# Performance work log

Measured on AMD Instinct MI355X. Metric: run time of the kernel, lower is better.

Reference implementation:

```python
import jax, jax.numpy as jnp
import numpy as np

MIN_EXPERT_CAPACITY = 4
CAPACITY_FACTOR = 1.0


def setup_inputs() -> dict:
    key = jax.random.key(0)
    k0, k1, k2, k3 = jax.random.split(key, 4)
    B, S, D, E, F = 4, 2048, 1024, 8, 4096
    x = jax.random.normal(k0, (B, S, D), dtype=jnp.float32)
    router_w = jax.random.normal(k1, (D, E), dtype=jnp.float32) * (D ** -0.5)
    w1 = jax.random.normal(k2, (E, D, F), dtype=jnp.float32) * (D ** -0.5)
    b1 = jnp.zeros((E, F), dtype=jnp.float32)
    w2 = jax.random.normal(k3, (E, F, D), dtype=jnp.float32) * (F ** -0.5)
    b2 = jnp.zeros((E, D), dtype=jnp.float32)
    return {"x": x, "router_w": router_w, "w1": w1, "b1": b1, "w2": w2, "b2": b2}


def _moe_forward(x, router_w, w1, b1, w2, b2):
    B, S, D = x.shape
    E = router_w.shape[1]
    G = 1  # num_groups (single device -> all-to-all is identity)
    T = B * S  # tokens per group
    C = max(int(round(CAPACITY_FACTOR * T / E)), MIN_EXPERT_CAPACITY)

    xt = x.reshape(G, T, D)
    # ---- top-1 tokens-choose masked router ----
    logits = jnp.einsum('gtd,de->gte', xt, router_w)
    probs = jax.nn.softmax(logits, axis=-1)
    gate = jnp.max(probs, axis=-1)          # [g, t]
    idx = jnp.argmax(probs, axis=-1)        # [g, t]
    emask = jax.nn.one_hot(idx, E, dtype=x.dtype)  # [g, t, e]
    # position of each token within its chosen expert's buffer (0-based);
    # -1 for unselected slots -> one_hot gives zeros
    pos = jnp.cumsum(emask, axis=1) * emask - 1.0
    pos = pos.astype(jnp.int32)
    # drop tokens beyond capacity
    slot = jax.nn.one_hot(pos, C, dtype=x.dtype)   # [g, t, e, c]
    dispatch = emask[..., None] * slot             # [g, t, e, c] (0/1)
    combine = dispatch * gate[..., None, None]     # [g, t, e, c]

    # ---- dispatch / expert FFN / combine ----
    expert_inputs = jnp.einsum('gtd,gtec->gecd', xt, dispatch)        # [g, e, c, d]
    h = jax.nn.relu(jnp.einsum('gecd,edf->gecf', expert_inputs, w1) + b1[None, :, None, :])
    expert_outputs = jnp.einsum('gecf,efd->gecd', h, w2) + b2[None, :, None, :]
    out = jnp.einsum('gecd,gtec->gtd', expert_outputs, combine)       # [g, t, d]
    return out.reshape(B, S, D)


def reference(x, router_w, w1, b1, w2, b2):
    return _moe_forward(x, router_w, w1, b1, w2, b2)
```

## Files before the change

kernel.cpp:

```cpp
#include <hip/hip_runtime.h>
#include <hip/hip_fp16.h>

typedef unsigned short ushort_t;
typedef __attribute__((ext_vector_type(8))) _Float16 half8v;
typedef __attribute__((ext_vector_type(4))) float float4v;
typedef __attribute__((ext_vector_type(8))) unsigned short ushort8v;

#define DEV_INLINE __device__ __forceinline__

DEV_INLINE ushort_t f2h_bits(float f) {
  return __half_as_ushort(__float2half(f));
}

__global__ __launch_bounds__(256) void router_kernel(
    const float* __restrict__ x, const float* __restrict__ rw,
    int* __restrict__ idx, float* __restrict__ gate)
{
  constexpr int D = 1024, E = 8;
  int token = (int)((blockIdx.x * 256 + threadIdx.x) >> 6);
  int lane = threadIdx.x & 63;
  const float* xr = x + (size_t)token * D;
  float acc[E];
#pragma unroll
  for (int e = 0; e < E; ++e) acc[e] = 0.f;
  for (int d = lane; d < D; d += 64) {
    float xv = xr[d];
#pragma unroll
    for (int e = 0; e < E; ++e) acc[e] += xv * rw[d * E + e];
  }
#pragma unroll
  for (int off = 32; off >= 1; off >>= 1) {
#pragma unroll
    for (int e = 0; e < E; ++e) acc[e] += __shfl_xor(acc[e], off);
  }
  if (lane == 0) {
    float m = acc[0]; int am = 0;
#pragma unroll
    for (int e = 1; e < E; ++e) { if (acc[e] > m) { m = acc[e]; am = e; } }
    float s = 0.f;
#pragma unroll
    for (int e = 0; e < E; ++e) s += __expf(acc[e] - m);
    idx[token] = am;
    gate[token] = 1.0f / s;
  }
}

__global__ __launch_bounds__(1024) void scan_kernel(
    const int* __restrict__ idx,
    int* __restrict__ slotmap, int* __restrict__ tok2slot)
{
  constexpr int C = 1024, E = 8;
  __shared__ unsigned long long s0[1024];
  __shared__ unsigned long long s1[1024];
  int tid = threadIdx.x;
  int myidx[8];
  unsigned long long c0 = 0, c1 = 0;
#pragma unroll
  for (int j = 0; j < 8; ++j) {
    int e = idx[tid * 8 + j];
    myidx[j] = e;
    if (e < 4) c0 += 1ull << (16 * e);
    else       c1 += 1ull << (16 * (e - 4));
  }
  s0[tid] = c0; s1[tid] = c1;
  __syncthreads();
  for (int off = 1; off < 1024; off <<= 1) {
    unsigned long long b0 = 0, b1 = 0;
    if (tid >= off) { b0 = s0[tid - off]; b1 = s1[tid - off]; }
    __syncthreads();
    s0[tid] += b0; s1[tid] += b1;
    __syncthreads();
  }
  unsigned long long p0 = s0[tid] - c0, p1 = s1[tid] - c1;
  unsigned long long t0 = s0[1023], t1 = s1[1023];
  int cnt[E];
#pragma unroll
  for (int e = 0; e < 4; ++e) {
    cnt[e]     = (int)((p0 >> (16 * e)) & 0xFFFF);
    cnt[4 + e] = (int)((p1 >> (16 * e)) & 0xFFFF);
  }
#pragma unroll
  for (int j = 0; j < 8; ++j) {
    int t = tid * 8 + j;
    int e = myidx[j];
    int pos = cnt[e]++;
    if (pos < C) {
      slotmap[e * C + pos] = t;
      tok2slot[t] = e * C + pos;
    } else {
      tok2slot[t] = -1;
    }
  }
  int total[E];
#pragma unroll
  for (int e = 0; e < 4; ++e) {
    total[e]     = (int)((t0 >> (16 * e)) & 0xFFFF);
    total[4 + e] = (int)((t1 >> (16 * e)) & 0xFFFF);
  }
  for (int s = tid; s < E * C; s += 1024) {
    int e = s / C, c = s % C;
    if (c >= total[e]) slotmap[s] = -1;
  }
}

__global__ __launch_bounds__(256) void gather_kernel(
    const float* __restrict__ x, const int* __restrict__ slotmap,
    ushort_t* __restrict__ Xe)
{
  constexpr int D = 1024;
  int slot = blockIdx.x;
  int t = slotmap[slot];
  int tid = threadIdx.x;
  ushort4* dst = (ushort4*)(Xe + (size_t)slot * D);
  ushort4 o;
  if (t >= 0) {
    float4 v = ((const float4*)(x + (size_t)t * D))[tid];
    o.x = f2h_bits(v.x); o.y = f2h_bits(v.y); o.z = f2h_bits(v.z); o.w = f2h_bits(v.w);
  } else {
    o.x = 0; o.y = 0; o.z = 0; o.w = 0;
  }
  dst[tid] = o;
}

__global__ __launch_bounds__(256) void transpose_cvt(
    const float* __restrict__ in, ushort_t* __restrict__ out, int R, int Cc)
{
  __shared__ ushort_t tile[64][65];
  size_t base = (size_t)blockIdx.z * (size_t)R * (size_t)Cc;
  int c0 = blockIdx.x * 64, r0 = blockIdx.y * 64;
  int tx = threadIdx.x & 63, ty = threadIdx.x >> 6;
#pragma unroll
  for (int i = 0; i < 16; ++i) {
    int r = ty + 4 * i;
    tile[r][tx] = f2h_bits(in[base + (size_t)(r0 + r) * Cc + c0 + tx]);
  }
  __syncthreads();
#pragma unroll
  for (int i = 0; i < 2; ++i) {
    int chunk = (int)threadIdx.x + i * 256;
    int c = chunk >> 3, g = chunk & 7;
    ushort8v v;
#pragma unroll
    for (int j = 0; j < 8; ++j) v[j] = tile[8 * g + j][c];
    *(ushort8v*)(out + base + (size_t)(c0 + c) * R + r0 + 8 * g) = v;
  }
}

__global__ __launch_bounds__(256) void combine_kernel(
    const float* __restrict__ p, const float* __restrict__ b2,
    const int* __restrict__ tok2slot, const float* __restrict__ gate,
    float* __restrict__ out)
{
  constexpr int D = 1024;
  constexpr size_t ECD = (size_t)8 * 1024 * 1024;
  int t = blockIdx.x;
  int d4 = threadIdx.x;
  float4* o = (float4*)(out + (size_t)t * D);
  int slot = tok2slot[t];
  if (slot < 0) { o[d4] = make_float4(0.f, 0.f, 0.f, 0.f); return; }
  int e = slot >> 10;
  float g = gate[t];
  float4 a = ((const float4*)(p + (size_t)slot * D))[d4];
  float4 b = ((const float4*)(p + ECD + (size_t)slot * D))[d4];
  float4 bb = ((const float4*)(b2 + (size_t)e * D))[d4];
  o[d4] = make_float4((a.x + b.x + bb.x) * g, (a.y + b.y + bb.y) * g,
                      (a.z + b.z + bb.z) * g, (a.w + b.w + bb.w) * g);
}

#define BAR()  asm volatile("s_barrier" ::: "memory")
#define VM2()  asm volatile("s_waitcnt vmcnt(2)" ::: "memory")
#define VM4()  asm volatile("s_waitcnt vmcnt(4)" ::: "memory")
#define VM0()  asm volatile("s_waitcnt vmcnt(0)" ::: "memory")

#define RD_A0(buf) { _Pragma("unroll") for (int i_ = 0; i_ < 4; ++i_) { \
  _Pragma("unroll") for (int kh_ = 0; kh_ < 2; ++kh_) \
    aS0[i_][kh_] = *(const half8v*)&lds[buf][kh_*KH + (arow + i_*16)*32 + axor]; } }
#define RD_A1(buf) { _Pragma("unroll") for (int i_ = 0; i_ < 4; ++i_) { \
  _Pragma("unroll") for (int kh_ = 0; kh_ < 2; ++kh_) \
    aS1[i_][kh_] = *(const half8v*)&lds[buf][kh_*KH + (arow + (4+i_)*16)*32 + axor]; } }
#define RD_B0(buf) { _Pragma("unroll") for (int j_ = 0; j_ < 2; ++j_) { \
  _Pragma("unroll") for (int kh_ = 0; kh_ < 2; ++kh_) \
    bS0[j_][kh_] = *(const half8v*)&lds[buf][AELEM + kh_*KH + (brow + j_*16)*32 + axor]; } }
#define RD_B1(buf) { _Pragma("unroll") for (int j_ = 0; j_ < 2; ++j_) { \
  _Pragma("unroll") for (int kh_ = 0; kh_ < 2; ++kh_) \
    bS1[j_][kh_] = *(const half8v*)&lds[buf][AELEM + kh_*KH + (brow + (2+j_)*16)*32 + axor]; } }

#define MQ(AS, BS, MB, NB) { __builtin_amdgcn_s_setprio(1); \
  _Pragma("unroll") for (int i_ = 0; i_ < 4; ++i_) { \
  _Pragma("unroll") for (int j_ = 0; j_ < 2; ++j_) { \
    acc[(MB)+i_][(NB)+j_] = __builtin_amdgcn_mfma_f32_16x16x32_f16(AS[i_][0], BS[j_][0], acc[(MB)+i_][(NB)+j_], 0, 0, 0); \
    acc[(MB)+i_][(NB)+j_] = __builtin_amdgcn_mfma_f32_16x16x32_f16(AS[i_][1], BS[j_][1], acc[(MB)+i_][(NB)+j_], 0, 0, 0); } } \
  __builtin_amdgcn_s_setprio(0); }

template<int KFULL, int NTM, int NTN, int SK, int MODE>
__global__ __launch_bounds__(512, 2) void gemm8p(
    const ushort_t* __restrict__ A, const ushort_t* __restrict__ Bt,
    const float* __restrict__ bias,
    ushort_t* __restrict__ Hout, float* __restrict__ outp)
{
  constexpr int M_ = NTM * 256, N_ = NTN * 256;
  constexpr int KB = KFULL / SK;
  constexpr int NT = KB / 64;
  constexpr int NU = NT / 2;
  constexpr int KH = 256 * 32;
  constexpr int AELEM = 2 * KH;
  constexpr int WPB = NTM * NTN * SK;
  constexpr int NWG = 8 * WPB;
  constexpr int CPX = NWG / 8;

  __shared__ __attribute__((aligned(16))) ushort_t lds[2][2 * AELEM];

  const int bid = blockIdx.x;
  const int swz = (bid & 7) * CPX + (bid >> 3);
  const int e   = swz / WPB;
  int r = swz % WPB;
  const int sk  = r / (NTM * NTN);  r %= NTM * NTN;
  const int nt  = r / NTM;
  const int mt  = r % NTM;
  const int kb0 = sk * KB;

  const ushort_t* Ae = A  + (size_t)e * M_ * KFULL + (size_t)(mt * 256) * KFULL + kb0;
  const ushort_t* Be = Bt + (size_t)e * N_ * KFULL + (size_t)(nt * 256) * KFULL + kb0;

  const int tid  = threadIdx.x;
  const int lane = tid & 63;
  const int w    = tid >> 6;
  const int wr   = w >> 2;
  const int wc   = w & 3;
  const int l15  = lane & 15;
  const int axor = ((lane >> 4) ^ ((l15 >> 1) & 3)) << 3;
  const int arow = wr * 128 + l15;
  const int brow = wc * 64 + l15;

  const int srow = tid >> 2;
  const int su   = tid & 3;
  auto stage = [&](int buf, int isB, int h, int ktile) {
    const ushort_t* base = isB ? Be : Ae;
#pragma unroll
    for (int kh = 0; kh < 2; ++kh) {
      int row = h * 128 + srow;
      int ul  = su ^ ((row >> 1) & 3);
      const ushort_t* src = base + (size_t)row * KFULL + ktile * 64 + kh * 32 + ul * 8;
      __builtin_amdgcn_global_load_lds(
          (const __attribute__((address_space(1))) void*)src,
          (__attribute__((address_space(3))) void*)(&lds[buf][isB * AELEM + kh * KH + h * 4096 + tid * 8]),
          16, 0, 0);
    }
  };

  float4v acc[8][4] = {};
  half8v aS0[4][2], aS1[4][2], bS0[2][2], bS1[2][2];

  stage(0, 0, 0, 0); stage(0, 0, 1, 0); stage(0, 1, 0, 0); stage(0, 1, 1, 0);
  stage(1, 1, 0, 1); stage(1, 0, 0, 1);
  VM4(); BAR();
  RD_A0(0); RD_B0(0);

  for (int u = 0; u < NU - 1; ++u) {
    const int t1 = 2 * u + 1, t2 = 2 * u + 2, t3 = 2 * u + 3;
    RD_B1(0); stage(1, 0, 1, t1); BAR(); MQ(aS0, bS0, 0, 0); BAR();
    RD_A1(0); stage(1, 1, 1, t1); BAR(); MQ(aS0, bS1, 0, 2); VM2(); BAR();
    RD_A0(1); stage(0, 1, 0, t2); BAR(); MQ(aS1, bS0, 4, 0); VM2(); BAR();
    RD_B0(1); stage(0, 0, 0, t2); BAR(); MQ(aS1, bS1, 4, 2); BAR();
    RD_B1(1); stage(0, 0, 1, t2); BAR(); MQ(aS0, bS0, 0, 0); BAR();
    RD_A1(1); stage(0, 1, 1, t2); BAR(); MQ(aS0, bS1, 0, 2); VM2(); BAR();
    RD_A0(0); stage(1, 1, 0, t3); BAR(); MQ(aS1, bS0, 4, 0); VM2(); BAR();
    RD_B0(0); stage(1, 0, 0, t3); BAR(); MQ(aS1, bS1, 4, 2); BAR();
  }
  {
    const int t1 = NT - 1;
    RD_B1(0); stage(1, 0, 1, t1); BAR(); MQ(aS0, bS0, 0, 0); BAR();
    RD_A1(0); stage(1, 1, 1, t1); BAR(); MQ(aS0, bS1, 0, 2); VM2(); BAR();
    RD_A0(1);                     BAR(); MQ(aS1, bS0, 4, 0); VM0(); BAR();
    RD_B0(1);                     BAR(); MQ(aS1, bS1, 4, 2); BAR();
    RD_B1(1);                     BAR(); MQ(aS0, bS0, 0, 0); BAR();
    RD_A1(1);                     BAR(); MQ(aS0, bS1, 0, 2); BAR();
                                  BAR(); MQ(aS1, bS0, 4, 0); BAR();
                                         MQ(aS1, bS1, 4, 2);
  }

  const int lr4   = (lane >> 4) * 4;
  const int mbase = mt * 256 + wr * 128;
  const int nbase = nt * 256 + wc * 64;

  if (MODE == 0) {
    float bv[4];
#pragma unroll
    for (int j = 0; j < 4; ++j) bv[j] = bias[e * N_ + nbase + j * 16 + l15];
    ushort_t* He = Hout + (size_t)e * M_ * N_;
#pragma unroll
    for (int i = 0; i < 8; ++i) {
#pragma unroll
      for (int q = 0; q < 4; ++q) {
        int m = mbase + i * 16 + lr4 + q;
#pragma unroll
        for (int j = 0; j < 4; ++j) {
          float v = acc[i][j][q] + bv[j];
          v = v > 0.f ? v : 0.f;
          He[(size_t)m * N_ + nbase + j * 16 + l15] = f2h_bits(v);
        }
      }
    }
  } else {
    float* pe = outp + ((size_t)(sk * 8 + e)) * (size_t)M_ * N_;
#pragma unroll
    for (int i = 0; i < 8; ++i) {
#pragma unroll
      for (int q = 0; q < 4; ++q) {
        int m = mbase + i * 16 + lr4 + q;
#pragma unroll
        for (int j = 0; j < 4; ++j) {
          pe[(size_t)m * N_ + nbase + j * 16 + l15] = acc[i][j][q];
        }
      }
    }
  }
}

extern "C" void kernel_launch(void* const* d_in, const int* in_sizes, int n_in,
                              void* d_out, int out_size, void* d_ws, size_t ws_size,
                              hipStream_t stream)
{
  const float* x  = (const float*)d_in[0];
  const float* rw = (const float*)d_in[1];
  const float* w1 = (const float*)d_in[2];
  const float* b1 = (const float*)d_in[3];
  const float* w2 = (const float*)d_in[4];
  const float* b2 = (const float*)d_in[5];
  float* out = (float*)d_out;

  constexpr int D = 1024, E = 8, F = 4096, T = 8192, C = 1024;

  char* p = (char*)d_ws;
  auto take = [&](size_t bytes) { char* r = p; p += (bytes + 255) & ~(size_t)255; return r; };
  ushort_t* w1t = (ushort_t*)take((size_t)E * D * F * 2);
  ushort_t* w2t = (ushort_t*)take((size_t)E * F * D * 2);
  ushort_t* Xe  = (ushort_t*)take((size_t)E * C * D * 2);
  ushort_t* H   = (ushort_t*)take((size_t)E * C * F * 2);
  int*      idx = (int*)take((size_t)T * 4);
  float*   gate = (float*)take((size_t)T * 4);
  int*  slotmap = (int*)take((size_t)E * C * 4);
  int* tok2slot = (int*)take((size_t)T * 4);

  float* partials = (float*)w1t;

  router_kernel<<<T / 4, 256, 0, stream>>>(x, rw, idx, gate);
  scan_kernel<<<1, 1024, 0, stream>>>(idx, slotmap, tok2slot);
  gather_kernel<<<E * C, 256, 0, stream>>>(x, slotmap, Xe);
  transpose_cvt<<<dim3(F / 64, D / 64, E), 256, 0, stream>>>(w1, w1t, D, F);
  transpose_cvt<<<dim3(D / 64, F / 64, E), 256, 0, stream>>>(w2, w2t, F, D);
  gemm8p<1024, 4, 16, 1, 0><<<512, 512, 0, stream>>>(Xe, w1t, b1, H, nullptr);
  gemm8p<4096, 4, 4, 2, 1><<<256, 512, 0, stream>>>(H, w2t, nullptr, nullptr, partials);
  combine_kernel<<<T, 256, 0, stream>>>(partials, b2, tok2slot, gate, out);
}
```

Before: 284.1 us.

## Reschedule GEMM LDS prefetch pipeline and merge weight transpose launches

Reorders the GEMM main loop so each phase reads both the A and B fragments from LDS together, then spreads the global-to-LDS staging across the MFMA phases. The prologue now prefetches three stages, and the vmcnt waits are loosened to allow 4–6 loads in flight, with lgkmcnt waits added. The aim is to hide global load latency behind MFMA work and cut barrier stalls. The two weight transpose/convert launches are also merged into one kernel to save a launch and its tail, at the cost of more register pressure and a more fragile hand-tuned wait schedule.

```diff
diff --git a/kernel.cpp b/kernel.cpp
--- a/kernel.cpp
+++ b/kernel.cpp
@@ -122,12 +122,23 @@
   dst[tid] = o;
 }
 
-__global__ __launch_bounds__(256) void transpose_cvt(
-    const float* __restrict__ in, ushort_t* __restrict__ out, int R, int Cc)
+__global__ __launch_bounds__(256) void transpose_cvt2(
+    const float* __restrict__ w1, ushort_t* __restrict__ w1t,
+    const float* __restrict__ w2, ushort_t* __restrict__ w2t)
 {
   __shared__ ushort_t tile[64][65];
-  size_t base = (size_t)blockIdx.z * (size_t)R * (size_t)Cc;
-  int c0 = blockIdx.x * 64, r0 = blockIdx.y * 64;
+  int bb = blockIdx.x;
+  const float* in; ushort_t* out; int R, Cc, bx, by, bz;
+  if (bb < 8192) {
+    in = w1; out = w1t; R = 1024; Cc = 4096;
+    bz = bb >> 10; int rr = bb & 1023; bx = rr & 63; by = rr >> 6;
+  } else {
+    bb -= 8192;
+    in = w2; out = w2t; R = 4096; Cc = 1024;
+    bz = bb >> 10; int rr = bb & 1023; bx = rr & 15; by = rr >> 4;
+  }
+  size_t base = (size_t)bz * (size_t)R * (size_t)Cc;
+  int c0 = bx * 64, r0 = by * 64;
   int tx = threadIdx.x & 63, ty = threadIdx.x >> 6;
 #pragma unroll
   for (int i = 0; i < 16; ++i) {
@@ -167,10 +178,11 @@
                       (a.z + b.z + bb.z) * g, (a.w + b.w + bb.w) * g);
 }
 
-#define BAR()  asm volatile("s_barrier" ::: "memory")
-#define VM2()  asm volatile("s_waitcnt vmcnt(2)" ::: "memory")
-#define VM4()  asm volatile("s_waitcnt vmcnt(4)" ::: "memory")
-#define VM0()  asm volatile("s_waitcnt vmcnt(0)" ::: "memory")
+#define BAR()   asm volatile("s_barrier" ::: "memory")
+#define LGKM0() asm volatile("s_waitcnt lgkmcnt(0)" ::: "memory")
+#define VM4()   asm volatile("s_waitcnt vmcnt(4)" ::: "memory")
+#define VM6()   asm volatile("s_waitcnt vmcnt(6)" ::: "memory")
+#define VM0()   asm volatile("s_waitcnt vmcnt(0)" ::: "memory")
 
 #define RD_A0(buf) { _Pragma("unroll") for (int i_ = 0; i_ < 4; ++i_) { \
   _Pragma("unroll") for (int kh_ = 0; kh_ < 2; ++kh_) \
@@ -252,31 +264,41 @@
   half8v aS0[4][2], aS1[4][2], bS0[2][2], bS1[2][2];
 
   stage(0, 0, 0, 0); stage(0, 0, 1, 0); stage(0, 1, 0, 0); stage(0, 1, 1, 0);
-  stage(1, 1, 0, 1); stage(1, 0, 0, 1);
-  VM4(); BAR();
-  RD_A0(0); RD_B0(0);
+  stage(1, 0, 0, 1); stage(1, 0, 1, 1); stage(1, 1, 0, 1);
+  VM6(); BAR();
+  RD_B0(0); RD_A0(0);
 
   for (int u = 0; u < NU - 1; ++u) {
     const int t1 = 2 * u + 1, t2 = 2 * u + 2, t3 = 2 * u + 3;
-    RD_B1(0); stage(1, 0, 1, t1); BAR(); MQ(aS0, bS0, 0, 0); BAR();
-    RD_A1(0); stage(1, 1, 1, t1); BAR(); MQ(aS0, bS1, 0, 2); VM2(); BAR();
-    RD_A0(1); stage(0, 1, 0, t2); BAR(); MQ(aS1, bS0, 4, 0); VM2(); BAR();
-    RD_B0(1); stage(0, 0, 0, t2); BAR(); MQ(aS1, bS1, 4, 2); BAR();
-    RD_B1(1); stage(0, 0, 1, t2); BAR(); MQ(aS0, bS0, 0, 0); BAR();
-    RD_A1(1); stage(0, 1, 1, t2); BAR(); MQ(aS0, bS1, 0, 2); VM2(); BAR();
-    RD_A0(0); stage(1, 1, 0, t3); BAR(); MQ(aS1, bS0, 4, 0); VM2(); BAR();
-    RD_B0(0); stage(1, 0, 0, t3); BAR(); MQ(aS1, bS1, 4, 2); BAR();
+    RD_B1(0); RD_A1(0); stage(1, 1, 1, t1);
+    BAR(); MQ(aS0, bS0, 0, 0); LGKM0(); BAR();
+    stage(0, 0, 0, t2);
+    BAR(); MQ(aS0, bS1, 0, 2); BAR();
+    stage(0, 0, 1, t2);
+    BAR(); MQ(aS1, bS0, 4, 0); VM4(); BAR();
+    RD_B0(1); RD_A0(1); stage(0, 1, 0, t2);
+    BAR(); MQ(aS1, bS1, 4, 2); BAR();
+    RD_B1(1); RD_A1(1); stage(0, 1, 1, t2);
+    BAR(); MQ(aS0, bS0, 0, 0); LGKM0(); BAR();
+    stage(1, 0, 0, t3);
+    BAR(); MQ(aS0, bS1, 0, 2); BAR();
+    stage(1, 0, 1, t3);
+    BAR(); MQ(aS1, bS0, 4, 0); VM4(); BAR();
+    RD_B0(0); RD_A0(0); stage(1, 1, 0, t3);
+    BAR(); MQ(aS1, bS1, 4, 2); BAR();
   }
   {
-    const int t1 = NT - 1;
-    RD_B1(0); stage(1, 0, 1, t1); BAR(); MQ(aS0, bS0, 0, 0); BAR();
-    RD_A1(0); stage(1, 1, 1, t1); BAR(); MQ(aS0, bS1, 0, 2); VM2(); BAR();
-    RD_A0(1);                     BAR(); MQ(aS1, bS0, 4, 0); VM0(); BAR();
-    RD_B0(1);                     BAR(); MQ(aS1, bS1, 4, 2); BAR();
-    RD_B1(1);                     BAR(); MQ(aS0, bS0, 0, 0); BAR();
-    RD_A1(1);                     BAR(); MQ(aS0, bS1, 0, 2); BAR();
-                                  BAR(); MQ(aS1, bS0, 4, 0); BAR();
-                                         MQ(aS1, bS1, 4, 2);
+    RD_B1(0); RD_A1(0); stage(1, 1, 1, NT - 1);
+    BAR(); MQ(aS0, bS0, 0, 0); LGKM0(); BAR();
+    BAR(); MQ(aS0, bS1, 0, 2); BAR();
+    BAR(); MQ(aS1, bS0, 4, 0); VM0(); BAR();
+    RD_B0(1); RD_A0(1);
+    BAR(); MQ(aS1, bS1, 4, 2); BAR();
+    RD_B1(1); RD_A1(1);
+    BAR(); MQ(aS0, bS0, 0, 0); BAR();
+    BAR(); MQ(aS0, bS1, 0, 2); BAR();
+    BAR(); MQ(aS1, bS0, 4, 0); BAR();
+    MQ(aS1, bS1, 4, 2);
   }
 
   const int lr4   = (lane >> 4) * 4;
@@ -347,8 +369,7 @@
   router_kernel<<<T / 4, 256, 0, stream>>>(x, rw, idx, gate);
   scan_kernel<<<1, 1024, 0, stream>>>(idx, slotmap, tok2slot);
   gather_kernel<<<E * C, 256, 0, stream>>>(x, slotmap, Xe);
-  transpose_cvt<<<dim3(F / 64, D / 64, E), 256, 0, stream>>>(w1, w1t, D, F);
-  transpose_cvt<<<dim3(D / 64, F / 64, E), 256, 0, stream>>>(w2, w2t, F, D);
+  transpose_cvt2<<<16384, 256, 0, stream>>>(w1, w1t, w2, w2t);
   gemm8p<1024, 4, 16, 1, 0><<<512, 512, 0, stream>>>(Xe, w1t, b1, H, nullptr);
   gemm8p<4096, 4, 4, 2, 1><<<256, 512, 0, stream>>>(H, w2t, nullptr, nullptr, partials);
   combine_kernel<<<T, 256, 0, stream>>>(partials, b2, tok2slot, gate, out);
```

Result: faster. 277.6 us (-2.3%).

## Fuse weight fp32-to-fp16 transpose into GEMM B-tile loading

Applied to the files above, without the earlier changes.

Removes the two separate transpose_cvt kernels that converted and transposed w1 and w2 into fp16 workspace buffers. The GEMM now reads the fp32 weights directly through registers, converts them to fp16 and writes them transposed and swizzled into LDS, while A tiles still use direct global-to-LDS loads. The pipeline schedule is reworked around this register staging, with extra vmcnt(0) and lgkmcnt waits. This saves an extra full read and write pass over the weights, but the GEMM now reads twice as many bytes for B and adds VALU conversion and LDS-write work that may stall the MFMA pipeline.

```diff
diff --git a/kernel.cpp b/kernel.cpp
--- a/kernel.cpp
+++ b/kernel.cpp
@@ -10,6 +10,10 @@
 
 DEV_INLINE ushort_t f2h_bits(float f) {
   return __half_as_ushort(__float2half(f));
+}
+
+DEV_INLINE float comp4(const float4& q, int c) {
+  return c == 0 ? q.x : c == 1 ? q.y : c == 2 ? q.z : q.w;
 }
 
 __global__ __launch_bounds__(256) void router_kernel(
@@ -120,30 +124,6 @@
     o.x = 0; o.y = 0; o.z = 0; o.w = 0;
   }
   dst[tid] = o;
-}
-
-__global__ __launch_bounds__(256) void transpose_cvt(
-    const float* __restrict__ in, ushort_t* __restrict__ out, int R, int Cc)
-{
-  __shared__ ushort_t tile[64][65];
-  size_t base = (size_t)blockIdx.z * (size_t)R * (size_t)Cc;
-  int c0 = blockIdx.x * 64, r0 = blockIdx.y * 64;
-  int tx = threadIdx.x & 63, ty = threadIdx.x >> 6;
-#pragma unroll
-  for (int i = 0; i < 16; ++i) {
-    int r = ty + 4 * i;
-    tile[r][tx] = f2h_bits(in[base + (size_t)(r0 + r) * Cc + c0 + tx]);
-  }
-  __syncthreads();
-#pragma unroll
-  for (int i = 0; i < 2; ++i) {
-    int chunk = (int)threadIdx.x + i * 256;
-    int c = chunk >> 3, g = chunk & 7;
-    ushort8v v;
-#pragma unroll
-    for (int j = 0; j < 8; ++j) v[j] = tile[8 * g + j][c];
-    *(ushort8v*)(out + base + (size_t)(c0 + c) * R + r0 + 8 * g) = v;
-  }
 }
 
 __global__ __launch_bounds__(256) void combine_kernel(
@@ -167,10 +147,9 @@
                       (a.z + b.z + bb.z) * g, (a.w + b.w + bb.w) * g);
 }
 
-#define BAR()  asm volatile("s_barrier" ::: "memory")
-#define VM2()  asm volatile("s_waitcnt vmcnt(2)" ::: "memory")
-#define VM4()  asm volatile("s_waitcnt vmcnt(4)" ::: "memory")
-#define VM0()  asm volatile("s_waitcnt vmcnt(0)" ::: "memory")
+#define BAR()   asm volatile("s_barrier" ::: "memory")
+#define LGKM0() asm volatile("s_waitcnt lgkmcnt(0)" ::: "memory")
+#define VM0()   asm volatile("s_waitcnt vmcnt(0)" ::: "memory")
 
 #define RD_A0(buf) { _Pragma("unroll") for (int i_ = 0; i_ < 4; ++i_) { \
   _Pragma("unroll") for (int kh_ = 0; kh_ < 2; ++kh_) \
@@ -194,7 +173,7 @@
 
 template<int KFULL, int NTM, int NTN, int SK, int MODE>
 __global__ __launch_bounds__(512, 2) void gemm8p(
-    const ushort_t* __restrict__ A, const ushort_t* __restrict__ Bt,
+    const ushort_t* __restrict__ A, const float* __restrict__ Bf,
     const float* __restrict__ bias,
     ushort_t* __restrict__ Hout, float* __restrict__ outp)
 {
@@ -219,8 +198,8 @@
   const int mt  = r % NTM;
   const int kb0 = sk * KB;
 
-  const ushort_t* Ae = A  + (size_t)e * M_ * KFULL + (size_t)(mt * 256) * KFULL + kb0;
-  const ushort_t* Be = Bt + (size_t)e * N_ * KFULL + (size_t)(nt * 256) * KFULL + kb0;
+  const ushort_t* Ae = A + (size_t)e * M_ * KFULL + (size_t)(mt * 256) * KFULL + kb0;
+  const float*    Be = Bf + (size_t)e * KFULL * N_ + (size_t)kb0 * N_ + nt * 256;
 
   const int tid  = threadIdx.x;
   const int lane = tid & 63;
@@ -234,49 +213,90 @@
 
   const int srow = tid >> 2;
   const int su   = tid & 3;
-  auto stage = [&](int buf, int isB, int h, int ktile) {
-    const ushort_t* base = isB ? Be : Ae;
+  auto stageA = [&](int buf, int h, int ktile) {
 #pragma unroll
     for (int kh = 0; kh < 2; ++kh) {
       int row = h * 128 + srow;
       int ul  = su ^ ((row >> 1) & 3);
-      const ushort_t* src = base + (size_t)row * KFULL + ktile * 64 + kh * 32 + ul * 8;
+      const ushort_t* src = Ae + (size_t)row * KFULL + ktile * 64 + kh * 32 + ul * 8;
       __builtin_amdgcn_global_load_lds(
           (const __attribute__((address_space(1))) void*)src,
-          (__attribute__((address_space(3))) void*)(&lds[buf][isB * AELEM + kh * KH + h * 4096 + tid * 8]),
+          (__attribute__((address_space(3))) void*)(&lds[buf][kh * KH + h * 4096 + tid * 8]),
           16, 0, 0);
+    }
+  };
+
+  const int kqB   = tid & 15;
+  const int noctB = tid >> 4;
+  const int khB   = kqB >> 3;
+  const int guB   = (kqB >> 1) & 3;
+  const int hfB   = kqB & 1;
+  const int nb8   = noctB * 8;
+  float4 bf[8];
+  auto iB = [&](int ktile) {
+#pragma unroll
+    for (int kk = 0; kk < 4; ++kk)
+#pragma unroll
+      for (int nn = 0; nn < 2; ++nn)
+        bf[kk * 2 + nn] = *(const float4*)&Be[(size_t)(ktile * 64 + kqB * 4 + kk) * N_ + nb8 + nn * 4];
+  };
+  auto wB = [&](int buf) {
+#pragma unroll
+    for (int nn = 0; nn < 8; ++nn) {
+      const int n = nb8 + nn;
+      const int q = nn >> 2, c = nn & 3;
+      ushort4 wv;
+      wv.x = f2h_bits(comp4(bf[0 + q], c));
+      wv.y = f2h_bits(comp4(bf[2 + q], c));
+      wv.z = f2h_bits(comp4(bf[4 + q], c));
+      wv.w = f2h_bits(comp4(bf[6 + q], c));
+      *(ushort4*)&lds[buf][AELEM + khB * KH + n * 32 + ((guB ^ ((n >> 1) & 3)) << 3) + hfB * 4] = wv;
     }
   };
 
   float4v acc[8][4] = {};
   half8v aS0[4][2], aS1[4][2], bS0[2][2], bS1[2][2];
 
-  stage(0, 0, 0, 0); stage(0, 0, 1, 0); stage(0, 1, 0, 0); stage(0, 1, 1, 0);
-  stage(1, 1, 0, 1); stage(1, 0, 0, 1);
-  VM4(); BAR();
-  RD_A0(0); RD_B0(0);
-
-  for (int u = 0; u < NU - 1; ++u) {
-    const int t1 = 2 * u + 1, t2 = 2 * u + 2, t3 = 2 * u + 3;
-    RD_B1(0); stage(1, 0, 1, t1); BAR(); MQ(aS0, bS0, 0, 0); BAR();
-    RD_A1(0); stage(1, 1, 1, t1); BAR(); MQ(aS0, bS1, 0, 2); VM2(); BAR();
-    RD_A0(1); stage(0, 1, 0, t2); BAR(); MQ(aS1, bS0, 4, 0); VM2(); BAR();
-    RD_B0(1); stage(0, 0, 0, t2); BAR(); MQ(aS1, bS1, 4, 2); BAR();
-    RD_B1(1); stage(0, 0, 1, t2); BAR(); MQ(aS0, bS0, 0, 0); BAR();
-    RD_A1(1); stage(0, 1, 1, t2); BAR(); MQ(aS0, bS1, 0, 2); VM2(); BAR();
-    RD_A0(0); stage(1, 1, 0, t3); BAR(); MQ(aS1, bS0, 4, 0); VM2(); BAR();
-    RD_B0(0); stage(1, 0, 0, t3); BAR(); MQ(aS1, bS1, 4, 2); BAR();
+  iB(0); stageA(0, 0, 0); stageA(0, 1, 0);
+  VM0(); wB(0);
+  iB(1); stageA(1, 0, 1); stageA(1, 1, 1);
+  VM0(); wB(1);
+  if (NT > 2) iB(2);
+  LGKM0(); BAR();
+  RD_B0(0); RD_A0(0);
+
+  for (int u = 0; u <= NU - 2; ++u) {
+    const int t2 = 2 * u + 2, t3 = 2 * u + 3;
+    RD_B1(0); RD_A1(0);
+    BAR(); MQ(aS0, bS0, 0, 0); LGKM0(); BAR();
+    VM0(); wB(0); stageA(0, 0, t2);
+    BAR(); MQ(aS0, bS1, 0, 2); LGKM0(); BAR();
+    stageA(0, 1, t2); iB(t3);
+    BAR(); MQ(aS1, bS0, 4, 0); BAR();
+    RD_B0(1); RD_A0(1);
+    BAR(); MQ(aS1, bS1, 4, 2); BAR();
+    RD_B1(1); RD_A1(1);
+    BAR(); MQ(aS0, bS0, 0, 0); LGKM0(); BAR();
+    VM0(); wB(1); stageA(1, 0, t3);
+    BAR(); MQ(aS0, bS1, 0, 2); LGKM0(); BAR();
+    stageA(1, 1, t3);
+    if (u < NU - 2) iB(2 * u + 4);
+    BAR(); MQ(aS1, bS0, 4, 0); BAR();
+    RD_B0(0); RD_A0(0);
+    BAR(); MQ(aS1, bS1, 4, 2); BAR();
   }
   {
-    const int t1 = NT - 1;
-    RD_B1(0); stage(1, 0, 1, t1); BAR(); MQ(aS0, bS0, 0, 0); BAR();
-    RD_A1(0); stage(1, 1, 1, t1); BAR(); MQ(aS0, bS1, 0, 2); VM2(); BAR();
-    RD_A0(1);                     BAR(); MQ(aS1, bS0, 4, 0); VM0(); BAR();
-    RD_B0(1);                     BAR(); MQ(aS1, bS1, 4, 2); BAR();
-    RD_B1(1);                     BAR(); MQ(aS0, bS0, 0, 0); BAR();
-    RD_A1(1);                     BAR(); MQ(aS0, bS1, 0, 2); BAR();
-                                  BAR(); MQ(aS1, bS0, 4, 0); BAR();
-                                         MQ(aS1, bS1, 4, 2);
+    RD_B1(0); RD_A1(0);
+    MQ(aS0, bS0, 0, 0);
+    MQ(aS0, bS1, 0, 2);
+    MQ(aS1, bS0, 4, 0);
+    MQ(aS1, bS1, 4, 2);
+    VM0(); BAR();
+    RD_B0(1); RD_A0(1); RD_B1(1); RD_A1(1);
+    MQ(aS0, bS0, 0, 0);
+    MQ(aS0, bS1, 0, 2);
+    MQ(aS1, bS0, 4, 0);
+    MQ(aS1, bS1, 4, 2);
   }
 
   const int lr4   = (lane >> 4) * 4;
@@ -333,23 +353,18 @@
 
   char* p = (char*)d_ws;
   auto take = [&](size_t bytes) { char* r = p; p += (bytes + 255) & ~(size_t)255; return r; };
-  ushort_t* w1t = (ushort_t*)take((size_t)E * D * F * 2);
-  ushort_t* w2t = (ushort_t*)take((size_t)E * F * D * 2);
-  ushort_t* Xe  = (ushort_t*)take((size_t)E * C * D * 2);
-  ushort_t* H   = (ushort_t*)take((size_t)E * C * F * 2);
-  int*      idx = (int*)take((size_t)T * 4);
-  float*   gate = (float*)take((size_t)T * 4);
-  int*  slotmap = (int*)take((size_t)E * C * 4);
-  int* tok2slot = (int*)take((size_t)T * 4);
-
-  float* partials = (float*)w1t;
+  ushort_t* Xe       = (ushort_t*)take((size_t)E * C * D * 2);
+  ushort_t* H        = (ushort_t*)take((size_t)E * C * F * 2);
+  float*    partials = (float*)take((size_t)2 * E * C * D * 4);
+  int*      idx      = (int*)take((size_t)T * 4);
+  float*    gate     = (float*)take((size_t)T * 4);
+  int*      slotmap  = (int*)take((size_t)E * C * 4);
+  int*      tok2slot = (int*)take((size_t)T * 4);
 
   router_kernel<<<T / 4, 256, 0, stream>>>(x, rw, idx, gate);
   scan_kernel<<<1, 1024, 0, stream>>>(idx, slotmap, tok2slot);
   gather_kernel<<<E * C, 256, 0, stream>>>(x, slotmap, Xe);
-  transpose_cvt<<<dim3(F / 64, D / 64, E), 256, 0, stream>>>(w1, w1t, D, F);
-  transpose_cvt<<<dim3(D / 64, F / 64, E), 256, 0, stream>>>(w2, w2t, F, D);
-  gemm8p<1024, 4, 16, 1, 0><<<512, 512, 0, stream>>>(Xe, w1t, b1, H, nullptr);
-  gemm8p<4096, 4, 4, 2, 1><<<256, 512, 0, stream>>>(H, w2t, nullptr, nullptr, partials);
+  gemm8p<1024, 4, 16, 1, 0><<<512, 512, 0, stream>>>(Xe, w1, b1, H, nullptr);
+  gemm8p<4096, 4, 4, 2, 1><<<256, 512, 0, stream>>>(H, w2, nullptr, nullptr, partials);
   combine_kernel<<<T, 256, 0, stream>>>(partials, b2, tok2slot, gate, out);
 }
```

New measurement: 711.7 us. +150.5%, slower.
